# Kernel optimization log

Measured on AMD Instinct MI355X. Metric: run time of the kernel, lower is better.

The kernel has to match this reference:

```python
import jax, jax.numpy as jnp
import numpy as np

L, D, H, HD, FF, V = 2, 2048, 16, 128, 8192, 32000
B, S = 1, 2048
EPS = 1e-6
THETA = 10000.0


def setup_inputs() -> dict:
    key = jax.random.key(0)
    ks = jax.random.split(key, 10)
    s = 0.02
    w = lambda k, shape: jax.random.normal(k, shape, jnp.float32) * s
    return {
        "x": jax.random.normal(ks[0], (B, S, D), jnp.float32),
        "Wq": w(ks[1], (L, D, D)),
        "Wk": w(ks[2], (L, D, D)),
        "Wv": w(ks[3], (L, D, D)),
        "Wo": w(ks[4], (L, D, D)),
        "Wg": w(ks[5], (L, D, FF)),
        "Wu": w(ks[6], (L, D, FF)),
        "Wd": w(ks[7], (L, FF, D)),
        "ln1": jnp.ones((L, D), jnp.float32),
        "ln2": jnp.ones((L, D), jnp.float32),
        "lnf": jnp.ones((D,), jnp.float32),
        "Whead": w(ks[8], (D, V)),
    }


def rmsnorm(x, w):
    var = jnp.mean(x * x, axis=-1, keepdims=True)
    return x * jax.lax.rsqrt(var + EPS) * w


def rope_tables(seq_len, dtype):
    # HF LLaMA RoPE: inv_freq over even dims, cos/sin duplicated along last axis
    inv_freq = 1.0 / (THETA ** (jnp.arange(0, HD, 2, dtype=jnp.float32) / HD))
    ang = jnp.arange(seq_len, dtype=jnp.float32)[:, None] * inv_freq[None, :]  # [S, HD/2]
    emb = jnp.concatenate([ang, ang], axis=-1)  # [S, HD]
    return jnp.cos(emb).astype(dtype), jnp.sin(emb).astype(dtype)


def rotate_half(x):
    x1, x2 = x[..., : HD // 2], x[..., HD // 2 :]
    return jnp.concatenate([-x2, x1], axis=-1)


def apply_rope(x, cos, sin):
    # x: [B, H, S, HD]; cos/sin: [S, HD]
    return x * cos[None, None] + rotate_half(x) * sin[None, None]


def forward(x, Wq, Wk, Wv, Wo, Wg, Wu, Wd, ln1, ln2, lnf, Whead):
    b, s, d = x.shape
    cos, sin = rope_tables(s, x.dtype)
    causal = jnp.tril(jnp.ones((s, s), dtype=bool))  # [S, S]
    neg = jnp.finfo(x.dtype).min
    scale = 1.0 / np.sqrt(HD)
    for l in range(L):
        # --- self attention (naive MATH SDPA: materialized scores) ---
        h = rmsnorm(x, ln1[l])
        q = (h @ Wq[l]).reshape(b, s, H, HD).transpose(0, 2, 1, 3)
        k = (h @ Wk[l]).reshape(b, s, H, HD).transpose(0, 2, 1, 3)
        v = (h @ Wv[l]).reshape(b, s, H, HD).transpose(0, 2, 1, 3)
        q = apply_rope(q, cos, sin)
        k = apply_rope(k, cos, sin)
        scores = jnp.einsum("bhqd,bhkd->bhqk", q, k) * scale
        scores = jnp.where(causal[None, None], scores, neg)
        attn = jax.nn.softmax(scores, axis=-1)
        o = jnp.einsum("bhqk,bhkd->bhqd", attn, v)
        o = o.transpose(0, 2, 1, 3).reshape(b, s, d) @ Wo[l]
        x = x + o
        # --- SwiGLU MLP ---
        h = rmsnorm(x, ln2[l])
        x = x + (jax.nn.silu(h @ Wg[l]) * (h @ Wu[l])) @ Wd[l]
    x = rmsnorm(x, lnf)
    return x @ Whead  # [B, S, V] logits


def reference(x, Wq, Wk, Wv, Wo, Wg, Wu, Wd, ln1, ln2, lnf, Whead):
    return forward(x, Wq, Wk, Wv, Wo, Wg, Wu, Wd, ln1, ln2, lnf, Whead)
```

## Files before the change

### kernel.cpp

```cpp
#include <hip/hip_runtime.h>
#include <hip/hip_bf16.h>
#include <stdint.h>

#define L_  2
#define D_  2048
#define H_  16
#define HD_ 128
#define FF_ 8192
#define V_  32000
#define S_  2048

typedef __attribute__((ext_vector_type(8))) short s8v;
typedef __attribute__((ext_vector_type(4))) short s4v;
typedef __attribute__((ext_vector_type(4))) float f4v;

__device__ __forceinline__ unsigned short f2bf(float x) {
  unsigned int u = __float_as_uint(x);
  u += 0x7fffu + ((u >> 16) & 1u);
  return (unsigned short)(u >> 16);
}

__device__ __forceinline__ void gload16(const void* g, void* l) {
  __builtin_amdgcn_global_load_lds((__attribute__((address_space(1))) const void*)g,
                                   (__attribute__((address_space(3))) void*)l, 16, 0, 0);
}

__global__ __launch_bounds__(256) void k_transpose(
    const float* __restrict__ src, unsigned short* __restrict__ dst,
    int srcld, int dstld, size_t src_z, size_t dst_z)
{
  __shared__ float ts[32][33];
  src += blockIdx.z * src_z;
  dst += blockIdx.z * dst_z;
  const int t  = threadIdx.x;
  const int r0 = blockIdx.y * 32, c0 = blockIdx.x * 32;
  const int lr = t >> 3, lc = (t & 7) * 4;
  float4 v = *(const float4*)(src + (size_t)(r0 + lr) * srcld + c0 + lc);
  ts[lr][lc + 0] = v.x; ts[lr][lc + 1] = v.y; ts[lr][lc + 2] = v.z; ts[lr][lc + 3] = v.w;
  __syncthreads();
  const int oc = t >> 3, orr = (t & 7) * 4;
  s4v o;
  o[0] = (short)f2bf(ts[orr + 0][oc]);
  o[1] = (short)f2bf(ts[orr + 1][oc]);
  o[2] = (short)f2bf(ts[orr + 2][oc]);
  o[3] = (short)f2bf(ts[orr + 3][oc]);
  *(s4v*)(dst + (size_t)(c0 + oc) * dstld + r0 + orr) = o;
}

__global__ __launch_bounds__(256) void k_rmsnorm(
    const float* __restrict__ x, const float* __restrict__ w,
    unsigned short* __restrict__ out)
{
  const int row = blockIdx.x, tid = threadIdx.x;
  const float4* x4 = (const float4*)(x + (size_t)row * D_);
  const float4* w4 = (const float4*)w;
  float4 v0 = x4[tid], v1 = x4[tid + 256];
  float s = v0.x*v0.x + v0.y*v0.y + v0.z*v0.z + v0.w*v0.w
          + v1.x*v1.x + v1.y*v1.y + v1.z*v1.z + v1.w*v1.w;
  #pragma unroll
  for (int o = 32; o; o >>= 1) s += __shfl_xor(s, o);
  __shared__ float red[4];
  if ((tid & 63) == 0) red[tid >> 6] = s;
  __syncthreads();
  float rs = rsqrtf((red[0] + red[1] + red[2] + red[3]) * (1.0f / D_) + 1e-6f);
  float4 wv = w4[tid];
  s4v o4;
  o4[0] = (short)f2bf(v0.x * rs * wv.x); o4[1] = (short)f2bf(v0.y * rs * wv.y);
  o4[2] = (short)f2bf(v0.z * rs * wv.z); o4[3] = (short)f2bf(v0.w * rs * wv.w);
  *(s4v*)(out + (size_t)row * D_ + tid * 4) = o4;
  wv = w4[tid + 256];
  o4[0] = (short)f2bf(v1.x * rs * wv.x); o4[1] = (short)f2bf(v1.y * rs * wv.y);
  o4[2] = (short)f2bf(v1.z * rs * wv.z); o4[3] = (short)f2bf(v1.w * rs * wv.w);
  *(s4v*)(out + (size_t)row * D_ + (tid + 256) * 4) = o4;
}

__global__ void k_rope_tab(float* __restrict__ cosT, float* __restrict__ sinT)
{
  int idx = blockIdx.x * 256 + threadIdx.x;
  int s = idx >> 6, d = idx & 63;
  float inv = powf(10000.0f, -(float)d * (1.0f / 64.0f));
  float ang = (float)s * inv;
  cosT[idx] = cosf(ang);
  sinT[idx] = sinf(ang);
}

__global__ void k_rope(const float* __restrict__ src, unsigned short* __restrict__ dst,
                       const float* __restrict__ cosT, const float* __restrict__ sinT,
                       int srcld, int colbase)
{
  int idx = blockIdx.x * 256 + threadIdx.x;
  int d = idx & 127;
  int s = (idx >> 7) & (S_ - 1);
  int h = idx >> 18;
  float v = src[(size_t)s * srcld + colbase + h * HD_ + d];
  float p = src[(size_t)s * srcld + colbase + h * HD_ + (d ^ 64)];
  float c  = cosT[s * 64 + (d & 63)];
  float sn = sinT[s * 64 + (d & 63)];
  float rot = (d < 64) ? -p : p;
  dst[idx] = f2bf(v * c + rot * sn);
}

template <int EPI>
__global__ __launch_bounds__(256) void k_gemm(
    const unsigned short* __restrict__ A, const unsigned short* __restrict__ Bt,
    float* __restrict__ C, unsigned short* __restrict__ Cb,
    const float* __restrict__ aux, int M, int N, int K)
{
  __shared__ short As[128 * 32];
  __shared__ short Bs[128 * 32];
  const int tid  = threadIdx.x;
  const int lane = tid & 63;
  const int w    = tid >> 6;
  const int wr = w >> 1, wc = w & 1;
  const int g = lane >> 4, q = lane & 15;
  const int brow = blockIdx.y * 128;
  const int bcol = blockIdx.x * 128;

  const int srow = w * 16 + (lane >> 2);
  const int sk   = (lane & 3) * 8;
  const unsigned short* gA = A  + (size_t)(brow + srow) * K + sk;
  const unsigned short* gB = Bt + (size_t)(bcol + srow) * K + sk;
  char* lA = (char*)As + w * 1024;
  char* lB = (char*)Bs + w * 1024;

  f4v acc[4][4];
  #pragma unroll
  for (int m = 0; m < 4; m++)
    #pragma unroll
    for (int n = 0; n < 4; n++) acc[m][n] = (f4v){0.f, 0.f, 0.f, 0.f};

  for (int k0 = 0; k0 < K; k0 += 32) {
    gload16(gA + k0,                    lA);
    gload16(gA + (size_t)64 * K + k0,   lA + 4096);
    gload16(gB + k0,                    lB);
    gload16(gB + (size_t)64 * K + k0,   lB + 4096);
    __syncthreads();
    s8v a[4], b[4];
    #pragma unroll
    for (int m = 0; m < 4; m++) a[m] = *(const s8v*)(As + (wr * 64 + m * 16 + q) * 32 + g * 8);
    #pragma unroll
    for (int n = 0; n < 4; n++) b[n] = *(const s8v*)(Bs + (wc * 64 + n * 16 + q) * 32 + g * 8);
    #pragma unroll
    for (int m = 0; m < 4; m++)
      #pragma unroll
      for (int n = 0; n < 4; n++)
        acc[m][n] = __builtin_amdgcn_mfma_f32_16x16x32_bf16(a[m], b[n], acc[m][n], 0, 0, 0);
    __syncthreads();
  }

  #pragma unroll
  for (int m = 0; m < 4; m++) {
    const size_t row0 = (size_t)brow + wr * 64 + m * 16 + g * 4;
    #pragma unroll
    for (int n = 0; n < 4; n++) {
      const size_t col = (size_t)bcol + wc * 64 + n * 16 + q;
      f4v v = acc[m][n];
      #pragma unroll
      for (int i = 0; i < 4; i++) {
        size_t idx = (row0 + i) * (size_t)N + col;
        if (EPI == 0) {
          C[idx] = v[i];
        } else if (EPI == 1) {
          C[idx] += v[i];
        } else {
          float gv = aux[idx];
          float sv = gv / (1.0f + __expf(-gv));
          Cb[idx] = f2bf(sv * v[i]);
        }
      }
    }
  }
}

__global__ __launch_bounds__(64) void k_flash(
    const unsigned short* __restrict__ qb, const unsigned short* __restrict__ kb,
    const unsigned short* __restrict__ vT, unsigned short* __restrict__ outp)
{
  const int lane = threadIdx.x;
  const int g = lane >> 4, q = lane & 15;
  const int qt = blockIdx.x, h = blockIdx.y;
  const int qrow = qt * 16 + q;
  const unsigned short* Qh = qb + ((size_t)h * S_ + (size_t)qt * 16) * HD_;
  const unsigned short* Kh = kb + (size_t)h * S_ * HD_;
  const unsigned short* Vh = vT + (size_t)h * HD_ * S_;

  s8v qf[4];
  #pragma unroll
  for (int c = 0; c < 4; c++)
    qf[c] = *(const s8v*)(Qh + q * HD_ + c * 32 + g * 8);

  f4v o[8];
  #pragma unroll
  for (int dt = 0; dt < 8; dt++) o[dt] = (f4v){0.f, 0.f, 0.f, 0.f};
  float mrun = -1e30f, lrun = 0.f;
  const float scale = 0.08838834764831845f;
  const int addr0 = (((g & 1) * 2) * 16 + q) * 4;
  const int addr1 = addr0 + 64;
  const bool thi = (g >> 1) != 0;

  for (int jb = 0; jb <= qt * 16 + 15; jb += 32) {
    f4v st[2] = {(f4v){0.f,0.f,0.f,0.f}, (f4v){0.f,0.f,0.f,0.f}};
    #pragma unroll
    for (int t2 = 0; t2 < 2; t2++)
      #pragma unroll
      for (int c = 0; c < 4; c++) {
        s8v kf = *(const s8v*)(Kh + (size_t)(jb + t2 * 16 + q) * HD_ + c * 32 + g * 8);
        st[t2] = __builtin_amdgcn_mfma_f32_16x16x32_bf16(kf, qf[c], st[t2], 0, 0, 0);
      }
    float pm = -1e30f;
    float p[2][4];
    #pragma unroll
    for (int t2 = 0; t2 < 2; t2++)
      #pragma unroll
      for (int r = 0; r < 4; r++) {
        int key = jb + t2 * 16 + g * 4 + r;
        float v = st[t2][r] * scale;
        v = (key <= qrow) ? v : -1e30f;
        p[t2][r] = v;
        pm = fmaxf(pm, v);
      }
    pm = fmaxf(pm, __shfl_xor(pm, 16));
    pm = fmaxf(pm, __shfl_xor(pm, 32));
    float mnew  = fmaxf(mrun, pm);
    float alpha = __expf(mrun - mnew);
    float ls = 0.f;
    #pragma unroll
    for (int t2 = 0; t2 < 2; t2++)
      #pragma unroll
      for (int r = 0; r < 4; r++) { float e = __expf(p[t2][r] - mnew); p[t2][r] = e; ls += e; }
    ls += __shfl_xor(ls, 16);
    ls += __shfl_xor(ls, 32);
    lrun = lrun * alpha + ls;
    mrun = mnew;
    #pragma unroll
    for (int dt = 0; dt < 8; dt++) o[dt] *= alpha;

    unsigned int pk00 = (unsigned)f2bf(p[0][0]) | ((unsigned)f2bf(p[0][1]) << 16);
    unsigned int pk01 = (unsigned)f2bf(p[0][2]) | ((unsigned)f2bf(p[0][3]) << 16);
    unsigned int pk10 = (unsigned)f2bf(p[1][0]) | ((unsigned)f2bf(p[1][1]) << 16);
    unsigned int pk11 = (unsigned)f2bf(p[1][2]) | ((unsigned)f2bf(p[1][3]) << 16);
    int b00 = __builtin_amdgcn_ds_bpermute(addr0, (int)pk00);
    int b01 = __builtin_amdgcn_ds_bpermute(addr0, (int)pk01);
    int b02 = __builtin_amdgcn_ds_bpermute(addr1, (int)pk00);
    int b03 = __builtin_amdgcn_ds_bpermute(addr1, (int)pk01);
    int b10 = __builtin_amdgcn_ds_bpermute(addr0, (int)pk10);
    int b11 = __builtin_amdgcn_ds_bpermute(addr0, (int)pk11);
    int b12 = __builtin_amdgcn_ds_bpermute(addr1, (int)pk10);
    int b13 = __builtin_amdgcn_ds_bpermute(addr1, (int)pk11);
    union { int wds[4]; s8v s; } pf;
    pf.wds[0] = thi ? b10 : b00;
    pf.wds[1] = thi ? b11 : b01;
    pf.wds[2] = thi ? b12 : b02;
    pf.wds[3] = thi ? b13 : b03;

    #pragma unroll
    for (int dt = 0; dt < 8; dt++) {
      s8v vf = *(const s8v*)(Vh + (size_t)(dt * 16 + q) * S_ + jb + g * 8);
      o[dt] = __builtin_amdgcn_mfma_f32_16x16x32_bf16(vf, pf.s, o[dt], 0, 0, 0);
    }
  }

  float inv_l = 1.0f / lrun;
  #pragma unroll
  for (int dt = 0; dt < 8; dt++)
    #pragma unroll
    for (int r = 0; r < 4; r++) {
      float val = o[dt][r] * inv_l;
      outp[(size_t)(qt * 16 + q) * D_ + h * HD_ + dt * 16 + g * 4 + r] = f2bf(val);
    }
}

extern "C" void kernel_launch(void* const* d_in, const int* in_sizes, int n_in,
                              void* d_out, int out_size, void* d_ws, size_t ws_size,
                              hipStream_t stream)
{
  (void)in_sizes; (void)n_in; (void)out_size;
  const float* x_in = (const float*)d_in[0];
  const float* Wq   = (const float*)d_in[1];
  const float* Wk   = (const float*)d_in[2];
  const float* Wv   = (const float*)d_in[3];
  const float* Wo   = (const float*)d_in[4];
  const float* Wg   = (const float*)d_in[5];
  const float* Wu   = (const float*)d_in[6];
  const float* Wd   = (const float*)d_in[7];
  const float* ln1  = (const float*)d_in[8];
  const float* ln2  = (const float*)d_in[9];
  const float* lnf  = (const float*)d_in[10];
  const float* Wh   = (const float*)d_in[11];

  char* ws = (char*)d_ws;
  size_t off = 0;
  auto alloc = [&](size_t bytes) -> void* {
    void* p = ws + off;
    off += (bytes + 255) & ~(size_t)255;
    return p;
  };
  float*          x     = (float*)         alloc((size_t)S_ * D_ * 4);
  unsigned short* hbuf  = (unsigned short*)alloc((size_t)S_ * D_ * 2);
  float*          cosT  = (float*)         alloc((size_t)S_ * 64 * 4);
  float*          sinT  = (float*)         alloc((size_t)S_ * 64 * 4);
  size_t wT_layer = (size_t)4 * D_ * D_ + 3 * (size_t)FF_ * D_;
  size_t wT_head  = (size_t)V_ * D_;
  size_t wT_elems = wT_layer > wT_head ? wT_layer : wT_head;
  unsigned short* wT    = (unsigned short*)alloc(wT_elems * 2);
  char*           sc    = (char*)          alloc((size_t)96 * 1024 * 1024);
  if (ws_size < off) return;

  float*          qkv   = (float*)         (sc);
  unsigned short* qbb   = (unsigned short*)(sc + (size_t)48 * 1048576);
  unsigned short* kbb   = (unsigned short*)(sc + (size_t)56 * 1048576);
  unsigned short* vT    = (unsigned short*)(sc + (size_t)64 * 1048576);
  unsigned short* attno = (unsigned short*)(sc + (size_t)72 * 1048576);
  float*          gbuf  = (float*)         (sc);
  unsigned short* act   = (unsigned short*)(sc + (size_t)64 * 1048576);

  unsigned short* WqT = wT;
  unsigned short* WkT = WqT + (size_t)D_ * D_;
  unsigned short* WvT = WkT + (size_t)D_ * D_;
  unsigned short* WoT = WvT + (size_t)D_ * D_;
  unsigned short* WgT = WoT + (size_t)D_ * D_;
  unsigned short* WuT = WgT + (size_t)FF_ * D_;
  unsigned short* WdT = WuT + (size_t)FF_ * D_;

  auto tr = [&](const float* s, unsigned short* d, int rows, int cols) {
    dim3 gr(cols / 32, rows / 32, 1);
    hipLaunchKernelGGL(k_transpose, gr, dim3(256), 0, stream, s, d, cols, rows, (size_t)0, (size_t)0);
  };
  auto gemm = [&](int epi, const unsigned short* A, const unsigned short* Bt,
                  float* C, unsigned short* Cb, const float* aux, int M, int N, int K) {
    dim3 gr(N / 128, M / 128, 1);
    if (epi == 0)      hipLaunchKernelGGL(k_gemm<0>, gr, dim3(256), 0, stream, A, Bt, C, Cb, aux, M, N, K);
    else if (epi == 1) hipLaunchKernelGGL(k_gemm<1>, gr, dim3(256), 0, stream, A, Bt, C, Cb, aux, M, N, K);
    else               hipLaunchKernelGGL(k_gemm<2>, gr, dim3(256), 0, stream, A, Bt, C, Cb, aux, M, N, K);
  };

  hipMemcpyAsync(x, x_in, (size_t)S_ * D_ * 4, hipMemcpyDeviceToDevice, stream);
  hipLaunchKernelGGL(k_rope_tab, dim3((S_ * 64) / 256), dim3(256), 0, stream, cosT, sinT);

  for (int l = 0; l < L_; l++) {
    tr(Wq + (size_t)l * D_ * D_,  WqT, D_,  D_);
    tr(Wk + (size_t)l * D_ * D_,  WkT, D_,  D_);
    tr(Wv + (size_t)l * D_ * D_,  WvT, D_,  D_);
    tr(Wo + (size_t)l * D_ * D_,  WoT, D_,  D_);
    tr(Wg + (size_t)l * D_ * FF_, WgT, D_,  FF_);
    tr(Wu + (size_t)l * D_ * FF_, WuT, D_,  FF_);
    tr(Wd + (size_t)l * FF_ * D_, WdT, FF_, D_);

    hipLaunchKernelGGL(k_rmsnorm, dim3(S_), dim3(256), 0, stream, x, ln1 + (size_t)l * D_, hbuf);
    gemm(0, hbuf, WqT, qkv, nullptr, nullptr, S_, 3 * D_, D_);

    hipLaunchKernelGGL(k_rope, dim3((H_ * S_ * HD_) / 256), dim3(256), 0, stream,
                       qkv, qbb, cosT, sinT, 3 * D_, 0);
    hipLaunchKernelGGL(k_rope, dim3((H_ * S_ * HD_) / 256), dim3(256), 0, stream,
                       qkv, kbb, cosT, sinT, 3 * D_, D_);
    hipLaunchKernelGGL(k_transpose, dim3(HD_ / 32, S_ / 32, H_), dim3(256), 0, stream,
                       qkv + 2 * D_, vT, 3 * D_, S_, (size_t)HD_, (size_t)HD_ * S_);

    hipLaunchKernelGGL(k_flash, dim3(S_ / 16, H_), dim3(64), 0, stream, qbb, kbb, vT, attno);

    gemm(1, attno, WoT, x, nullptr, nullptr, S_, D_, D_);

    hipLaunchKernelGGL(k_rmsnorm, dim3(S_), dim3(256), 0, stream, x, ln2 + (size_t)l * D_, hbuf);
    gemm(0, hbuf, WgT, gbuf, nullptr, nullptr, S_, FF_, D_);
    gemm(2, hbuf, WuT, nullptr, act, gbuf,    S_, FF_, D_);
    gemm(1, act, WdT, x, nullptr, nullptr,    S_, D_, FF_);
  }

  hipLaunchKernelGGL(k_rmsnorm, dim3(S_), dim3(256), 0, stream, x, lnf, hbuf);
  tr(Wh, wT, D_, V_);
  gemm(0, hbuf, wT, (float*)d_out, nullptr, nullptr, S_, V_, D_);
}
```

Before: 2.910 ms.

## Add XCD-aware tile remapping and split-K with atomics for residual GEMMs

Remaps the flat workgroup ID so that consecutive tiles land on the same XCD in column-major order, aiming to improve L2 reuse of shared A/B panels across the 8 XCDs. Adds a split-K mode via gridDim.z, used for the Wo (2-way) and Wd (4-way) residual GEMMs, where partial sums are accumulated into x with float atomicAdd. These two GEMMs launch only 256 tiles, so split-K is meant to fill more CUs. The cost is atomic traffic and nondeterministic summation order in the residual.

```diff
diff --git a/kernel.cpp b/kernel.cpp
--- a/kernel.cpp
+++ b/kernel.cpp
@@ -113,13 +113,23 @@
   const int w    = tid >> 6;
   const int wr = w >> 1, wc = w & 1;
   const int g = lane >> 4, q = lane & 15;
-  const int brow = blockIdx.y * 128;
-  const int bcol = blockIdx.x * 128;
+
+  const int nbx = gridDim.x, nby = gridDim.y;
+  const int nwg = nbx * nby;
+  const int flat = blockIdx.y * nbx + blockIdx.x;
+  const int qd = nwg >> 3, rm = nwg & 7;
+  const int xcd = flat & 7, id8 = flat >> 3;
+  const int wgid = (xcd < rm ? xcd * (qd + 1) : rm * (qd + 1) + (xcd - rm) * qd) + id8;
+  const int brow = (wgid % nby) * 128;
+  const int bcol = (wgid / nby) * 128;
+
+  const int Ks   = K / gridDim.z;
+  const int kbeg = blockIdx.z * Ks;
 
   const int srow = w * 16 + (lane >> 2);
   const int sk   = (lane & 3) * 8;
-  const unsigned short* gA = A  + (size_t)(brow + srow) * K + sk;
-  const unsigned short* gB = Bt + (size_t)(bcol + srow) * K + sk;
+  const unsigned short* gA = A  + (size_t)(brow + srow) * K + kbeg + sk;
+  const unsigned short* gB = Bt + (size_t)(bcol + srow) * K + kbeg + sk;
   char* lA = (char*)As + w * 1024;
   char* lB = (char*)Bs + w * 1024;
 
@@ -129,7 +139,7 @@
     #pragma unroll
     for (int n = 0; n < 4; n++) acc[m][n] = (f4v){0.f, 0.f, 0.f, 0.f};
 
-  for (int k0 = 0; k0 < K; k0 += 32) {
+  for (int k0 = 0; k0 < Ks; k0 += 32) {
     gload16(gA + k0,                    lA);
     gload16(gA + (size_t)64 * K + k0,   lA + 4096);
     gload16(gB + k0,                    lB);
@@ -161,7 +171,8 @@
         if (EPI == 0) {
           C[idx] = v[i];
         } else if (EPI == 1) {
-          C[idx] += v[i];
+          if (gridDim.z > 1) atomicAdd(&C[idx], v[i]);
+          else               C[idx] += v[i];
         } else {
           float gv = aux[idx];
           float sv = gv / (1.0f + __expf(-gv));
@@ -327,8 +338,9 @@
     hipLaunchKernelGGL(k_transpose, gr, dim3(256), 0, stream, s, d, cols, rows, (size_t)0, (size_t)0);
   };
   auto gemm = [&](int epi, const unsigned short* A, const unsigned short* Bt,
-                  float* C, unsigned short* Cb, const float* aux, int M, int N, int K) {
-    dim3 gr(N / 128, M / 128, 1);
+                  float* C, unsigned short* Cb, const float* aux,
+                  int M, int N, int K, int kz) {
+    dim3 gr(N / 128, M / 128, kz);
     if (epi == 0)      hipLaunchKernelGGL(k_gemm<0>, gr, dim3(256), 0, stream, A, Bt, C, Cb, aux, M, N, K);
     else if (epi == 1) hipLaunchKernelGGL(k_gemm<1>, gr, dim3(256), 0, stream, A, Bt, C, Cb, aux, M, N, K);
     else               hipLaunchKernelGGL(k_gemm<2>, gr, dim3(256), 0, stream, A, Bt, C, Cb, aux, M, N, K);
@@ -347,7 +359,7 @@
     tr(Wd + (size_t)l * FF_ * D_, WdT, FF_, D_);
 
     hipLaunchKernelGGL(k_rmsnorm, dim3(S_), dim3(256), 0, stream, x, ln1 + (size_t)l * D_, hbuf);
-    gemm(0, hbuf, WqT, qkv, nullptr, nullptr, S_, 3 * D_, D_);
+    gemm(0, hbuf, WqT, qkv, nullptr, nullptr, S_, 3 * D_, D_, 1);
 
     hipLaunchKernelGGL(k_rope, dim3((H_ * S_ * HD_) / 256), dim3(256), 0, stream,
                        qkv, qbb, cosT, sinT, 3 * D_, 0);
@@ -358,15 +370,15 @@
 
     hipLaunchKernelGGL(k_flash, dim3(S_ / 16, H_), dim3(64), 0, stream, qbb, kbb, vT, attno);
 
-    gemm(1, attno, WoT, x, nullptr, nullptr, S_, D_, D_);
+    gemm(1, attno, WoT, x, nullptr, nullptr, S_, D_, D_, 2);
 
     hipLaunchKernelGGL(k_rmsnorm, dim3(S_), dim3(256), 0, stream, x, ln2 + (size_t)l * D_, hbuf);
-    gemm(0, hbuf, WgT, gbuf, nullptr, nullptr, S_, FF_, D_);
-    gemm(2, hbuf, WuT, nullptr, act, gbuf,    S_, FF_, D_);
-    gemm(1, act, WdT, x, nullptr, nullptr,    S_, D_, FF_);
+    gemm(0, hbuf, WgT, gbuf, nullptr, nullptr, S_, FF_, D_, 1);
+    gemm(2, hbuf, WuT, nullptr, act, gbuf,    S_, FF_, D_, 1);
+    gemm(1, act, WdT, x, nullptr, nullptr,    S_, D_, FF_, 4);
   }
 
   hipLaunchKernelGGL(k_rmsnorm, dim3(S_), dim3(256), 0, stream, x, lnf, hbuf);
   tr(Wh, wT, D_, V_);
-  gemm(0, hbuf, wT, (float*)d_out, nullptr, nullptr, S_, V_, D_);
-}
+  gemm(0, hbuf, wT, (float*)d_out, nullptr, nullptr, S_, V_, D_, 1);
+}
```

After: 2.853 ms. -2.0%, faster.
